# Kernel optimization log

Measured on AMD Instinct MI355X. Metric: run time of the kernel, lower is better.

The kernel has to match this reference:

```python
import jax, jax.numpy as jnp
import numpy as np

NEG_SLOPE = 0.2

def gat_conv(x, edge_index, W, a_src, a_dst, b, heads, out_ch, concat):
    # PyG GATConv (add_self_loops=True, eval mode / no dropout)
    N = x.shape[0]
    loop = jnp.arange(N, dtype=edge_index.dtype)
    src = jnp.concatenate([edge_index[0], loop])
    dst = jnp.concatenate([edge_index[1], loop])
    h = (x @ W.T).reshape(N, heads, out_ch)            # [N,H,C]
    alpha_s = (h * a_src).sum(-1)                      # [N,H]
    alpha_d = (h * a_dst).sum(-1)                      # [N,H]
    e = jax.nn.leaky_relu(alpha_s[src] + alpha_d[dst], NEG_SLOPE)  # [E,H]
    # segment softmax over incoming edges of each dst node
    m = jax.ops.segment_max(e, dst, num_segments=N)
    e = jnp.exp(e - m[dst])
    denom = jax.ops.segment_sum(e, dst, num_segments=N)
    alpha = e / (denom[dst] + 1e-16)                   # [E,H]
    msg = h[src] * alpha[..., None]                    # [E,H,C]
    out = jax.ops.segment_sum(msg, dst, num_segments=N)  # [N,H,C]
    out = out.reshape(N, heads * out_ch) if concat else out.mean(axis=1)
    return out + b


def setup_inputs() -> dict:
    key = jax.random.key(0)
    ks = jax.random.split(key, 16)
    N, E, F_in, HID, H, OUT = 20000, 320000, 512, 256, 8, 128
    C = HID // H  # 32 channels per head
    x = jax.random.normal(ks[0], (N, F_in), dtype=jnp.float32)
    edge_index = jax.random.randint(ks[1], (2, E), 0, N, dtype=jnp.int32)
    s = 0.05
    inp = {
        'x': x, 'edge_index': edge_index,
        # layer 0: F_in -> H*C, concat
        'W0': jax.random.normal(ks[2], (H * C, F_in)) * s,
        'a_src0': jax.random.normal(ks[3], (1, H, C)) * s,
        'a_dst0': jax.random.normal(ks[4], (1, H, C)) * s,
        'b0': jnp.zeros((H * C,), jnp.float32),
        # layer 1: H*C -> H*C, concat
        'W1': jax.random.normal(ks[5], (H * C, H * C)) * s,
        'a_src1': jax.random.normal(ks[6], (1, H, C)) * s,
        'a_dst1': jax.random.normal(ks[7], (1, H, C)) * s,
        'b1': jnp.zeros((H * C,), jnp.float32),
        # layer 2: H*C -> OUT, 1 head, concat=False
        'W2': jax.random.normal(ks[8], (OUT, H * C)) * s,
        'a_src2': jax.random.normal(ks[9], (1, 1, OUT)) * s,
        'a_dst2': jax.random.normal(ks[10], (1, 1, OUT)) * s,
        'b2': jnp.zeros((OUT,), jnp.float32),
    }
    return inp


def reference(x, edge_index, W0, a_src0, a_dst0, b0, W1, a_src1, a_dst1, b1,
              W2, a_src2, a_dst2, b2):
    H, C, OUT = 8, 32, 128
    h = gat_conv(x, edge_index, W0, a_src0, a_dst0, b0, H, C, True)
    h = jax.nn.relu(h)
    h = gat_conv(h, edge_index, W1, a_src1, a_dst1, b1, H, C, True)
    h = jax.nn.relu(h)
    h_pen = h  # h_list[-1]
    h = gat_conv(h, edge_index, W2, a_src2, a_dst2, b2, 1, OUT, False)
    return (h_pen, h)
```

## Files before the change

kernel.cpp:

```cpp
#include <hip/hip_runtime.h>
#include <hip/hip_bf16.h>


using bf16 = __hip_bfloat16;

typedef __attribute__((ext_vector_type(8))) short bf16x8;
typedef __attribute__((ext_vector_type(4))) short short4v;
typedef __attribute__((ext_vector_type(4))) float f32x4;
typedef __attribute__((ext_vector_type(2))) float f32x2;
typedef __attribute__((ext_vector_type(2))) unsigned int uint2v;

__device__ __forceinline__ float u2f(unsigned u) { union { float f; unsigned u; } c; c.u = u; return c.f; }
__device__ __forceinline__ unsigned f2u(float x) { union { float f; unsigned u; } c; c.f = x; return c.u; }
__device__ __forceinline__ short bfbits(float x) {
  unsigned xu = f2u(x);
  return (short)((xu + 0x7FFF + ((xu >> 16) & 1)) >> 16);
}

__global__ void hist_kernel(const int* __restrict__ ei, int E, int N, int* __restrict__ cnt) {
  int e = blockIdx.x * 256 + threadIdx.x;
  if (e >= E + N) return;
  int dst = (e < E) ? ei[E + e] : (e - E);
  atomicAdd(&cnt[dst], 1);
}

__global__ __launch_bounds__(1024) void scan_kernel(const int* __restrict__ cnt,
                                                    int* __restrict__ row_start, int N) {
  __shared__ int part[1024];
  int t = threadIdx.x;
  int chunk = (N + 1023) / 1024;
  int lo = t * chunk; if (lo > N) lo = N;
  int hi = lo + chunk; if (hi > N) hi = N;
  int s = 0;
  for (int i = lo; i < hi; ++i) s += cnt[i];
  part[t] = s;
  __syncthreads();
  for (int off = 1; off < 1024; off <<= 1) {
    int add = (t >= off) ? part[t - off] : 0;
    __syncthreads();
    part[t] += add;
    __syncthreads();
  }
  int run = part[t] - s;
  for (int i = lo; i < hi; ++i) { row_start[i] = run; run += cnt[i]; }
  if (t == 1023) row_start[N] = part[1023];
}

__global__ void scatter_kernel(const int* __restrict__ ei, int E, int N,
                               const int* __restrict__ row_start, int* __restrict__ cursor,
                               int* __restrict__ csr_src) {
  int e = blockIdx.x * 256 + threadIdx.x;
  if (e >= E + N) return;
  int src, dst;
  if (e < E) { src = ei[e]; dst = ei[E + e]; }
  else       { src = e - E; dst = e - E; }
  int pos = atomicAdd(&cursor[dst], 1);
  csr_src[row_start[dst] + pos] = src;
}

__global__ void split_kernel(const float* __restrict__ in, unsigned short* __restrict__ hi,
                             unsigned short* __restrict__ lo, long long n4) {
  long long i = (long long)blockIdx.x * 256 + threadIdx.x;
  if (i >= n4) return;
  f32x4 v = *(const f32x4*)(in + i * 4);
  short4v h, l;
#pragma unroll
  for (int k = 0; k < 4; ++k) {
    short hb = bfbits(v[k]);
    h[k] = hb;
    l[k] = bfbits(v[k] - u2f(((unsigned)(unsigned short)hb) << 16));
  }
  *(short4v*)(hi + i * 4) = h;
  *(short4v*)(lo + i * 4) = l;
}

#define LDP 40

__device__ __forceinline__ bf16x8 make_frag(const short* S, int row, int g) {
  short4v klo = *(const short4v*)&S[row * LDP + g * 4];
  short4v khi = *(const short4v*)&S[row * LDP + 16 + g * 4];
  bf16x8 r;
#pragma unroll
  for (int i = 0; i < 4; ++i) { r[i] = klo[i]; r[i + 4] = khi[i]; }
  return r;
}

template <bool ASPLIT>
__global__ __launch_bounds__(256) void gemm_mfma(const float* __restrict__ Af,
                                                 const unsigned short* __restrict__ Ahg,
                                                 const unsigned short* __restrict__ Alg,
                                                 const unsigned short* __restrict__ Bhg,
                                                 const unsigned short* __restrict__ Blg,
                                                 float* __restrict__ C,
                                                 unsigned short* __restrict__ C16,
                                                 int M, int Nn, int K, int NB) {
  int id = blockIdx.x;
  int r8 = id & 7;
  int q  = id >> 3;
  int bn = q % NB;
  int bm = r8 + 8 * (q / NB);
  if (bm * 64 >= M) return;

  __shared__ short Ah[64 * LDP];
  __shared__ short Al[64 * LDP];
  __shared__ short Bh[64 * LDP];
  __shared__ short Bl[64 * LDP];
  int t = threadIdx.x;
  int w = t >> 6, l = t & 63;
  int g = l >> 4, lr = l & 15;

  f32x4 acc[4];
#pragma unroll
  for (int j = 0; j < 4; ++j) acc[j] = (f32x4)(0.f);

  int srow = t >> 2, sseg = t & 3;
  int gm = bm * 64 + srow;
  int gn = bn * 64 + srow;

  for (int kt = 0; kt < K; kt += 32) {
    __syncthreads();
    {
      size_t boff = (size_t)gn * K + kt + sseg * 8;
      int4 vh = *(const int4*)(Bhg + boff);
      int4 vl = *(const int4*)(Blg + boff);
      *(int4*)&Bh[srow * LDP + sseg * 8] = vh;
      *(int4*)&Bl[srow * LDP + sseg * 8] = vl;
    }
    if constexpr (ASPLIT) {
      f32x4 v0 = (f32x4)(0.f), v1 = (f32x4)(0.f);
      if (gm < M) {
        const float* Arow = Af + (size_t)gm * K + kt + sseg * 8;
        v0 = *(const f32x4*)Arow;
        v1 = *(const f32x4*)(Arow + 4);
      }
      short4v h0, l0, h1, l1;
#pragma unroll
      for (int i = 0; i < 4; ++i) {
        short hb0 = bfbits(v0[i]);
        l0[i] = bfbits(v0[i] - u2f(((unsigned)(unsigned short)hb0) << 16));
        h0[i] = hb0;
        short hb1 = bfbits(v1[i]);
        l1[i] = bfbits(v1[i] - u2f(((unsigned)(unsigned short)hb1) << 16));
        h1[i] = hb1;
      }
      *(short4v*)&Ah[srow * LDP + sseg * 8]     = h0;
      *(short4v*)&Ah[srow * LDP + sseg * 8 + 4] = h1;
      *(short4v*)&Al[srow * LDP + sseg * 8]     = l0;
      *(short4v*)&Al[srow * LDP + sseg * 8 + 4] = l1;
    } else {
      int4 vh = make_int4(0, 0, 0, 0), vl = make_int4(0, 0, 0, 0);
      if (gm < M) {
        size_t aoff = (size_t)gm * K + kt + sseg * 8;
        vh = *(const int4*)(Ahg + aoff);
        vl = *(const int4*)(Alg + aoff);
      }
      *(int4*)&Ah[srow * LDP + sseg * 8] = vh;
      *(int4*)&Al[srow * LDP + sseg * 8] = vl;
    }
    __syncthreads();

    int arow = w * 16 + lr;
    bf16x8 ah = make_frag(Ah, arow, g);
    bf16x8 al = make_frag(Al, arow, g);
#pragma unroll
    for (int j = 0; j < 4; ++j) {
      int brow = j * 16 + lr;
      bf16x8 bh = make_frag(Bh, brow, g);
      bf16x8 bl = make_frag(Bl, brow, g);
      acc[j] = __builtin_amdgcn_mfma_f32_16x16x32_bf16(ah, bh, acc[j], 0, 0, 0);
      acc[j] = __builtin_amdgcn_mfma_f32_16x16x32_bf16(al, bh, acc[j], 0, 0, 0);
      acc[j] = __builtin_amdgcn_mfma_f32_16x16x32_bf16(ah, bl, acc[j], 0, 0, 0);
    }
  }

#pragma unroll
  for (int j = 0; j < 4; ++j) {
#pragma unroll
    for (int r = 0; r < 4; ++r) {
      int row = bm * 64 + w * 16 + g * 4 + r;
      int col = bn * 64 + j * 16 + lr;
      if (row < M) {
        float v = acc[j][r];
        C[(size_t)row * Nn + col] = v;
        C16[(size_t)row * Nn + col] = (unsigned short)bfbits(v);
      }
    }
  }
}

template <int H, int C>
__global__ __launch_bounds__(64) void alpha_kernel(const float* __restrict__ Hb,
                                                   const float* __restrict__ a_src,
                                                   const float* __restrict__ a_dst,
                                                   float* __restrict__ as_,
                                                   float* __restrict__ ad_, int N) {
  constexpr int HC = H * C;
  constexpr int EPL = HC / 64;
  constexpr int LPH = 64 / H;
  int n = blockIdx.x;
  int l = threadIdx.x;
  const float* row = Hb + (size_t)n * HC + l * EPL;
  float s1 = 0.f, s2 = 0.f;
  if constexpr (EPL == 4) {
    f32x4 v = *(const f32x4*)row;
    f32x4 a1 = *(const f32x4*)(a_src + l * 4);
    f32x4 a2 = *(const f32x4*)(a_dst + l * 4);
#pragma unroll
    for (int k = 0; k < 4; ++k) { s1 += v[k] * a1[k]; s2 += v[k] * a2[k]; }
  } else {
    f32x2 v = *(const f32x2*)row;
    f32x2 a1 = *(const f32x2*)(a_src + l * 2);
    f32x2 a2 = *(const f32x2*)(a_dst + l * 2);
#pragma unroll
    for (int k = 0; k < 2; ++k) { s1 += v[k] * a1[k]; s2 += v[k] * a2[k]; }
  }
#pragma unroll
  for (int mask = 1; mask < LPH; mask <<= 1) {
    s1 += __shfl_xor(s1, mask);
    s2 += __shfl_xor(s2, mask);
  }
  if ((l & (LPH - 1)) == 0) {
    int h = l / LPH;
    as_[n * H + h] = s1;
    ad_[n * H + h] = s2;
  }
}

template <int H, int C, bool RELU>
__global__ __launch_bounds__(64) void agg_kernel(const unsigned short* __restrict__ Hb16,
                                                 const float* __restrict__ as_,
                                                 const float* __restrict__ ad_,
                                                 const int* __restrict__ row_start,
                                                 const int* __restrict__ csr_src,
                                                 const float* __restrict__ bias,
                                                 float* __restrict__ out_f,
                                                 unsigned short* __restrict__ out_h,
                                                 unsigned short* __restrict__ out_l,
                                                 int N) {
  int n = blockIdx.x;
  if (n >= N) return;
  int l = threadIdx.x;
  int s = row_start[n], e = row_start[n + 1];

  constexpr int LPH = 64 / H;
  constexpr int CPL = C / LPH;
  constexpr int HC = H * C;
  int h2 = l / LPH;
  int cb = (l % LPH) * CPL;
  float ad2 = ad_[n * H + h2];

  float acc[CPL];
#pragma unroll
  for (int c = 0; c < CPL; ++c) acc[c] = 0.f;
  float denom = 0.f;

  int j = s;
  for (; j + 1 < e; j += 2) {
    int s0 = csr_src[j], s1v = csr_src[j + 1];
    float x0 = as_[s0 * H + h2] + ad2;
    float x1 = as_[s1v * H + h2] + ad2;
    x0 = x0 > 0.f ? x0 : 0.2f * x0;
    x1 = x1 > 0.f ? x1 : 0.2f * x1;
    float p0 = __expf(x0), p1 = __expf(x1);
    denom += p0 + p1;
    const unsigned short* hp0 = Hb16 + (size_t)s0 * HC + h2 * C + cb;
    const unsigned short* hp1 = Hb16 + (size_t)s1v * HC + h2 * C + cb;
    if constexpr (CPL == 4) {
      uint2v u0 = *(const uint2v*)hp0;
      uint2v u1 = *(const uint2v*)hp1;
#pragma unroll
      for (int c = 0; c < 2; ++c) {
        acc[2 * c]     += p0 * u2f(u0[c] << 16)         + p1 * u2f(u1[c] << 16);
        acc[2 * c + 1] += p0 * u2f(u0[c] & 0xFFFF0000u) + p1 * u2f(u1[c] & 0xFFFF0000u);
      }
    } else {
      unsigned u0 = *(const unsigned*)hp0;
      unsigned u1 = *(const unsigned*)hp1;
      acc[0] += p0 * u2f(u0 << 16)         + p1 * u2f(u1 << 16);
      acc[1] += p0 * u2f(u0 & 0xFFFF0000u) + p1 * u2f(u1 & 0xFFFF0000u);
    }
  }
  if (j < e) {
    int s0 = csr_src[j];
    float x0 = as_[s0 * H + h2] + ad2;
    x0 = x0 > 0.f ? x0 : 0.2f * x0;
    float p0 = __expf(x0);
    denom += p0;
    const unsigned short* hp0 = Hb16 + (size_t)s0 * HC + h2 * C + cb;
    if constexpr (CPL == 4) {
      uint2v u0 = *(const uint2v*)hp0;
#pragma unroll
      for (int c = 0; c < 2; ++c) {
        acc[2 * c]     += p0 * u2f(u0[c] << 16);
        acc[2 * c + 1] += p0 * u2f(u0[c] & 0xFFFF0000u);
      }
    } else {
      unsigned u0 = *(const unsigned*)hp0;
      acc[0] += p0 * u2f(u0 << 16);
      acc[1] += p0 * u2f(u0 & 0xFFFF0000u);
    }
  }

  float inv = 1.f / (denom + 1e-16f);
#pragma unroll
  for (int c = 0; c < CPL; ++c) {
    float v = acc[c] * inv + bias[h2 * C + cb + c];
    if (RELU) v = fmaxf(v, 0.f);
    size_t oi = (size_t)n * HC + h2 * C + cb + c;
    if (out_f) out_f[oi] = v;
    if (out_h) {
      short hb = bfbits(v);
      out_h[oi] = (unsigned short)hb;
      out_l[oi] = (unsigned short)bfbits(v - u2f(((unsigned)(unsigned short)hb) << 16));
    }
  }
}

extern "C" void kernel_launch(void* const* d_in, const int* in_sizes, int n_in,
                              void* d_out, int out_size, void* d_ws, size_t ws_size,
                              hipStream_t stream) {
  const float* x    = (const float*)d_in[0];
  const int*   ei   = (const int*)d_in[1];
  const float* W0   = (const float*)d_in[2];
  const float* asr0 = (const float*)d_in[3];
  const float* adt0 = (const float*)d_in[4];
  const float* b0   = (const float*)d_in[5];
  const float* W1   = (const float*)d_in[6];
  const float* asr1 = (const float*)d_in[7];
  const float* adt1 = (const float*)d_in[8];
  const float* b1   = (const float*)d_in[9];
  const float* W2   = (const float*)d_in[10];
  const float* asr2 = (const float*)d_in[11];
  const float* adt2 = (const float*)d_in[12];
  const float* b2   = (const float*)d_in[13];

  const int FIN = 512, HID = 256, OUTC = 128;
  int N = in_sizes[0] / FIN;
  int E = in_sizes[1] / 2;
  int Etot = E + N;

  char* ws = (char*)d_ws;
  size_t off = 0;
  auto alloc = [&](size_t bytes) -> void* {
    void* p = ws + off;
    off = (off + bytes + 255) & ~(size_t)255;
    return p;
  };
  int* cnt       = (int*)alloc((size_t)N * 4);
  int* cursor    = (int*)alloc((size_t)N * 4);
  int* row_start = (int*)alloc((size_t)(N + 1) * 4);
  int* csr_src   = (int*)alloc((size_t)Etot * 4);
  float* as_     = (float*)alloc((size_t)N * 8 * 4);
  float* ad_     = (float*)alloc((size_t)N * 8 * 4);
  float* Hb      = (float*)alloc((size_t)N * HID * 4);
  unsigned short* Hb16  = (unsigned short*)alloc((size_t)N * HID * 2);
  unsigned short* act_h = (unsigned short*)alloc((size_t)N * HID * 2);
  unsigned short* act_l = (unsigned short*)alloc((size_t)N * HID * 2);
  unsigned short* h_h   = (unsigned short*)alloc((size_t)N * HID * 2);
  unsigned short* h_l   = (unsigned short*)alloc((size_t)N * HID * 2);
  unsigned short* W0h = (unsigned short*)alloc((size_t)HID * FIN * 2);
  unsigned short* W0l = (unsigned short*)alloc((size_t)HID * FIN * 2);
  unsigned short* W1h = (unsigned short*)alloc((size_t)HID * HID * 2);
  unsigned short* W1l = (unsigned short*)alloc((size_t)HID * HID * 2);
  unsigned short* W2h = (unsigned short*)alloc((size_t)OUTC * HID * 2);
  unsigned short* W2l = (unsigned short*)alloc((size_t)OUTC * HID * 2);

  float* hpen = (float*)d_out;
  float* out2 = (float*)d_out + (size_t)N * HID;

  long long w0n4 = (long long)HID * FIN / 4, w1n4 = (long long)HID * HID / 4,
            w2n4 = (long long)OUTC * HID / 4;
  split_kernel<<<(int)((w0n4 + 255) / 256), 256, 0, stream>>>(W0, W0h, W0l, w0n4);
  split_kernel<<<(int)((w1n4 + 255) / 256), 256, 0, stream>>>(W1, W1h, W1l, w1n4);
  split_kernel<<<(int)((w2n4 + 255) / 256), 256, 0, stream>>>(W2, W2h, W2l, w2n4);

  (void)hipMemsetAsync(cnt, 0, (size_t)N * 4, stream);
  (void)hipMemsetAsync(cursor, 0, (size_t)N * 4, stream);
  int eb = (Etot + 255) / 256;
  hist_kernel<<<eb, 256, 0, stream>>>(ei, E, N, cnt);
  scan_kernel<<<1, 1024, 0, stream>>>(cnt, row_start, N);
  scatter_kernel<<<eb, 256, 0, stream>>>(ei, E, N, row_start, cursor, csr_src);

  int mb = (N + 63) / 64;
  int mb8 = (mb + 7) / 8;
  int gemm_grid4 = 8 * 4 * mb8;
  int gemm_grid2 = 8 * 2 * mb8;

  gemm_mfma<true><<<gemm_grid4, 256, 0, stream>>>(x, nullptr, nullptr, W0h, W0l,
                                                  Hb, Hb16, N, HID, FIN, 4);
  alpha_kernel<8, 32><<<N, 64, 0, stream>>>(Hb, asr0, adt0, as_, ad_, N);
  agg_kernel<8, 32, true><<<N, 64, 0, stream>>>(Hb16, as_, ad_, row_start, csr_src, b0,
                                                nullptr, act_h, act_l, N);

  gemm_mfma<false><<<gemm_grid4, 256, 0, stream>>>(nullptr, act_h, act_l, W1h, W1l,
                                                   Hb, Hb16, N, HID, HID, 4);
  alpha_kernel<8, 32><<<N, 64, 0, stream>>>(Hb, asr1, adt1, as_, ad_, N);
  agg_kernel<8, 32, true><<<N, 64, 0, stream>>>(Hb16, as_, ad_, row_start, csr_src, b1,
                                                hpen, h_h, h_l, N);

  gemm_mfma<false><<<gemm_grid2, 256, 0, stream>>>(nullptr, h_h, h_l, W2h, W2l,
                                                   Hb, Hb16, N, OUTC, HID, 2);
  alpha_kernel<1, 128><<<N, 64, 0, stream>>>(Hb, asr2, adt2, as_, ad_, N);
  agg_kernel<1, 128, false><<<N, 64, 0, stream>>>(Hb16, as_, ad_, row_start, csr_src, b2,
                                                  out2, nullptr, nullptr, N);
}
```

Baseline: 256.7 us.

## Enlarge GEMM M-tile to 128 and split fp32 activations inside GEMM

The GEMM tile grows from 64x64 to 128x64, and each wave now computes a 64x32 sub-tile with 4x2 accumulators, so each loaded B fragment is reused across more A rows. The aggregation kernels now write plain fp32 activations instead of bf16 hi/lo pairs, and every GEMM splits A into hi/lo on the fly. This removes the separate split outputs and their memory traffic. The cost is more registers and LDS per block and half as many blocks.

```diff
diff --git a/kernel.cpp b/kernel.cpp
--- a/kernel.cpp
+++ b/kernel.cpp
@@ -74,21 +74,18 @@
   *(short4v*)(lo + i * 4) = l;
 }
 
-#define LDP 40
+#define LDPA 40
 
 __device__ __forceinline__ bf16x8 make_frag(const short* S, int row, int g) {
-  short4v klo = *(const short4v*)&S[row * LDP + g * 4];
-  short4v khi = *(const short4v*)&S[row * LDP + 16 + g * 4];
+  short4v klo = *(const short4v*)&S[row * LDPA + g * 4];
+  short4v khi = *(const short4v*)&S[row * LDPA + 16 + g * 4];
   bf16x8 r;
 #pragma unroll
   for (int i = 0; i < 4; ++i) { r[i] = klo[i]; r[i + 4] = khi[i]; }
   return r;
 }
 
-template <bool ASPLIT>
 __global__ __launch_bounds__(256) void gemm_mfma(const float* __restrict__ Af,
-                                                 const unsigned short* __restrict__ Ahg,
-                                                 const unsigned short* __restrict__ Alg,
                                                  const unsigned short* __restrict__ Bhg,
                                                  const unsigned short* __restrict__ Blg,
                                                  float* __restrict__ C,
@@ -99,37 +96,42 @@
   int q  = id >> 3;
   int bn = q % NB;
   int bm = r8 + 8 * (q / NB);
-  if (bm * 64 >= M) return;
-
-  __shared__ short Ah[64 * LDP];
-  __shared__ short Al[64 * LDP];
-  __shared__ short Bh[64 * LDP];
-  __shared__ short Bl[64 * LDP];
+  if (bm * 128 >= M) return;
+
+  __shared__ short Ah[128 * LDPA];
+  __shared__ short Al[128 * LDPA];
+  __shared__ short Bh[64 * LDPA];
+  __shared__ short Bl[64 * LDPA];
   int t = threadIdx.x;
   int w = t >> 6, l = t & 63;
   int g = l >> 4, lr = l & 15;
-
-  f32x4 acc[4];
-#pragma unroll
-  for (int j = 0; j < 4; ++j) acc[j] = (f32x4)(0.f);
-
-  int srow = t >> 2, sseg = t & 3;
-  int gm = bm * 64 + srow;
-  int gn = bn * 64 + srow;
+  int wm = w >> 1, wn = w & 1;
+
+  f32x4 acc[4][2];
+#pragma unroll
+  for (int a = 0; a < 4; ++a)
+#pragma unroll
+    for (int j = 0; j < 2; ++j) acc[a][j] = (f32x4)(0.f);
+
+  int srow = t >> 2;
+  int sseg = (t & 3) * 8;
 
   for (int kt = 0; kt < K; kt += 32) {
     __syncthreads();
     {
-      size_t boff = (size_t)gn * K + kt + sseg * 8;
+      size_t boff = (size_t)(bn * 64 + srow) * K + kt + sseg;
       int4 vh = *(const int4*)(Bhg + boff);
       int4 vl = *(const int4*)(Blg + boff);
-      *(int4*)&Bh[srow * LDP + sseg * 8] = vh;
-      *(int4*)&Bl[srow * LDP + sseg * 8] = vl;
-    }
-    if constexpr (ASPLIT) {
+      *(int4*)&Bh[srow * LDPA + sseg] = vh;
+      *(int4*)&Bl[srow * LDPA + sseg] = vl;
+    }
+#pragma unroll
+    for (int p = 0; p < 2; ++p) {
+      int arow = p * 64 + srow;
+      int gm = bm * 128 + arow;
       f32x4 v0 = (f32x4)(0.f), v1 = (f32x4)(0.f);
       if (gm < M) {
-        const float* Arow = Af + (size_t)gm * K + kt + sseg * 8;
+        const float* Arow = Af + (size_t)gm * K + kt + sseg;
         v0 = *(const f32x4*)Arow;
         v1 = *(const f32x4*)(Arow + 4);
       }
@@ -143,49 +145,50 @@
         l1[i] = bfbits(v1[i] - u2f(((unsigned)(unsigned short)hb1) << 16));
         h1[i] = hb1;
       }
-      *(short4v*)&Ah[srow * LDP + sseg * 8]     = h0;
-      *(short4v*)&Ah[srow * LDP + sseg * 8 + 4] = h1;
-      *(short4v*)&Al[srow * LDP + sseg * 8]     = l0;
-      *(short4v*)&Al[srow * LDP + sseg * 8 + 4] = l1;
-    } else {
-      int4 vh = make_int4(0, 0, 0, 0), vl = make_int4(0, 0, 0, 0);
-      if (gm < M) {
-        size_t aoff = (size_t)gm * K + kt + sseg * 8;
-        vh = *(const int4*)(Ahg + aoff);
-        vl = *(const int4*)(Alg + aoff);
-      }
-      *(int4*)&Ah[srow * LDP + sseg * 8] = vh;
-      *(int4*)&Al[srow * LDP + sseg * 8] = vl;
+      *(short4v*)&Ah[arow * LDPA + sseg]     = h0;
+      *(short4v*)&Ah[arow * LDPA + sseg + 4] = h1;
+      *(short4v*)&Al[arow * LDPA + sseg]     = l0;
+      *(short4v*)&Al[arow * LDPA + sseg + 4] = l1;
     }
     __syncthreads();
 
-    int arow = w * 16 + lr;
-    bf16x8 ah = make_frag(Ah, arow, g);
-    bf16x8 al = make_frag(Al, arow, g);
-#pragma unroll
-    for (int j = 0; j < 4; ++j) {
-      int brow = j * 16 + lr;
-      bf16x8 bh = make_frag(Bh, brow, g);
-      bf16x8 bl = make_frag(Bl, brow, g);
-      acc[j] = __builtin_amdgcn_mfma_f32_16x16x32_bf16(ah, bh, acc[j], 0, 0, 0);
-      acc[j] = __builtin_amdgcn_mfma_f32_16x16x32_bf16(al, bh, acc[j], 0, 0, 0);
-      acc[j] = __builtin_amdgcn_mfma_f32_16x16x32_bf16(ah, bl, acc[j], 0, 0, 0);
-    }
-  }
-
-#pragma unroll
-  for (int j = 0; j < 4; ++j) {
-#pragma unroll
-    for (int r = 0; r < 4; ++r) {
-      int row = bm * 64 + w * 16 + g * 4 + r;
-      int col = bn * 64 + j * 16 + lr;
-      if (row < M) {
-        float v = acc[j][r];
-        C[(size_t)row * Nn + col] = v;
-        C16[(size_t)row * Nn + col] = (unsigned short)bfbits(v);
-      }
-    }
-  }
+    bf16x8 ahf[4], alf[4], bhf[2], blf[2];
+#pragma unroll
+    for (int a = 0; a < 4; ++a) {
+      int arow = wm * 64 + a * 16 + lr;
+      ahf[a] = make_frag(Ah, arow, g);
+      alf[a] = make_frag(Al, arow, g);
+    }
+#pragma unroll
+    for (int j = 0; j < 2; ++j) {
+      int brow = wn * 32 + j * 16 + lr;
+      bhf[j] = make_frag(Bh, brow, g);
+      blf[j] = make_frag(Bl, brow, g);
+    }
+#pragma unroll
+    for (int a = 0; a < 4; ++a)
+#pragma unroll
+      for (int j = 0; j < 2; ++j) {
+        acc[a][j] = __builtin_amdgcn_mfma_f32_16x16x32_bf16(ahf[a], bhf[j], acc[a][j], 0, 0, 0);
+        acc[a][j] = __builtin_amdgcn_mfma_f32_16x16x32_bf16(alf[a], bhf[j], acc[a][j], 0, 0, 0);
+        acc[a][j] = __builtin_amdgcn_mfma_f32_16x16x32_bf16(ahf[a], blf[j], acc[a][j], 0, 0, 0);
+      }
+  }
+
+#pragma unroll
+  for (int a = 0; a < 4; ++a)
+#pragma unroll
+    for (int j = 0; j < 2; ++j)
+#pragma unroll
+      for (int r = 0; r < 4; ++r) {
+        int row = bm * 128 + wm * 64 + a * 16 + g * 4 + r;
+        int col = bn * 64 + wn * 32 + j * 16 + lr;
+        if (row < M) {
+          float v = acc[a][j][r];
+          C[(size_t)row * Nn + col] = v;
+          C16[(size_t)row * Nn + col] = (unsigned short)bfbits(v);
+        }
+      }
 }
 
 template <int H, int C>
@@ -233,10 +236,7 @@
                                                  const int* __restrict__ row_start,
                                                  const int* __restrict__ csr_src,
                                                  const float* __restrict__ bias,
-                                                 float* __restrict__ out_f,
-                                                 unsigned short* __restrict__ out_h,
-                                                 unsigned short* __restrict__ out_l,
-                                                 int N) {
+                                                 float* __restrict__ out, int N) {
   int n = blockIdx.x;
   if (n >= N) return;
   int l = threadIdx.x;
@@ -306,13 +306,7 @@
   for (int c = 0; c < CPL; ++c) {
     float v = acc[c] * inv + bias[h2 * C + cb + c];
     if (RELU) v = fmaxf(v, 0.f);
-    size_t oi = (size_t)n * HC + h2 * C + cb + c;
-    if (out_f) out_f[oi] = v;
-    if (out_h) {
-      short hb = bfbits(v);
-      out_h[oi] = (unsigned short)hb;
-      out_l[oi] = (unsigned short)bfbits(v - u2f(((unsigned)(unsigned short)hb) << 16));
-    }
+    out[(size_t)n * HC + h2 * C + cb + c] = v;
   }
 }
 
@@ -353,11 +347,8 @@
   float* as_     = (float*)alloc((size_t)N * 8 * 4);
   float* ad_     = (float*)alloc((size_t)N * 8 * 4);
   float* Hb      = (float*)alloc((size_t)N * HID * 4);
-  unsigned short* Hb16  = (unsigned short*)alloc((size_t)N * HID * 2);
-  unsigned short* act_h = (unsigned short*)alloc((size_t)N * HID * 2);
-  unsigned short* act_l = (unsigned short*)alloc((size_t)N * HID * 2);
-  unsigned short* h_h   = (unsigned short*)alloc((size_t)N * HID * 2);
-  unsigned short* h_l   = (unsigned short*)alloc((size_t)N * HID * 2);
+  unsigned short* Hb16 = (unsigned short*)alloc((size_t)N * HID * 2);
+  float* act     = (float*)alloc((size_t)N * HID * 4);
   unsigned short* W0h = (unsigned short*)alloc((size_t)HID * FIN * 2);
   unsigned short* W0l = (unsigned short*)alloc((size_t)HID * FIN * 2);
   unsigned short* W1h = (unsigned short*)alloc((size_t)HID * HID * 2);
@@ -381,26 +372,23 @@
   scan_kernel<<<1, 1024, 0, stream>>>(cnt, row_start, N);
   scatter_kernel<<<eb, 256, 0, stream>>>(ei, E, N, row_start, cursor, csr_src);
 
-  int mb = (N + 63) / 64;
+  int mb = (N + 127) / 128;
   int mb8 = (mb + 7) / 8;
-  int gemm_grid4 = 8 * 4 * mb8;
-  int gemm_grid2 = 8 * 2 * mb8;
-
-  gemm_mfma<true><<<gemm_grid4, 256, 0, stream>>>(x, nullptr, nullptr, W0h, W0l,
-                                                  Hb, Hb16, N, HID, FIN, 4);
+  int grid4 = 8 * 4 * mb8;
+  int grid2 = 8 * 2 * mb8;
+
+  gemm_mfma<<<grid4, 256, 0, stream>>>(x, W0h, W0l, Hb, Hb16, N, HID, FIN, 4);
   alpha_kernel<8, 32><<<N, 64, 0, stream>>>(Hb, asr0, adt0, as_, ad_, N);
   agg_kernel<8, 32, true><<<N, 64, 0, stream>>>(Hb16, as_, ad_, row_start, csr_src, b0,
-                                                nullptr, act_h, act_l, N);
-
-  gemm_mfma<false><<<gemm_grid4, 256, 0, stream>>>(nullptr, act_h, act_l, W1h, W1l,
-                                                   Hb, Hb16, N, HID, HID, 4);
+                                                act, N);
+
+  gemm_mfma<<<grid4, 256, 0, stream>>>(act, W1h, W1l, Hb, Hb16, N, HID, HID, 4);
   alpha_kernel<8, 32><<<N, 64, 0, stream>>>(Hb, asr1, adt1, as_, ad_, N);
   agg_kernel<8, 32, true><<<N, 64, 0, stream>>>(Hb16, as_, ad_, row_start, csr_src, b1,
-                                                hpen, h_h, h_l, N);
-
-  gemm_mfma<false><<<gemm_grid2, 256, 0, stream>>>(nullptr, h_h, h_l, W2h, W2l,
-                                                   Hb, Hb16, N, OUTC, HID, 2);
+                                                hpen, N);
+
+  gemm_mfma<<<grid2, 256, 0, stream>>>(hpen, W2h, W2l, Hb, Hb16, N, OUTC, HID, 2);
   alpha_kernel<1, 128><<<N, 64, 0, stream>>>(Hb, asr2, adt2, as_, ad_, N);
   agg_kernel<1, 128, false><<<N, 64, 0, stream>>>(Hb16, as_, ad_, row_start, csr_src, b2,
-                                                  out2, nullptr, nullptr, N);
-}
+                                                  out2, N);
+}
```

Result: faster. 248.1 us (-3.4%).
